# Optimization experiments

Hardware: AMD Instinct MI355X
Metric: run time of the kernel (lower is better)

The kernel has to match this reference:

```python
import jax, jax.numpy as jnp
import numpy as np

WIRES = 4

def _ry(theta):
    # theta: scalar or (N,) -> (2,2) or (N,2,2) complex64
    c = jnp.cos(theta / 2)
    s = jnp.sin(theta / 2)
    return jnp.stack([jnp.stack([c, -s], -1), jnp.stack([s, c], -1)], -2).astype(jnp.complex64)

def _rz(phi):
    e = jnp.exp(-0.5j * phi.astype(jnp.complex64))
    z = jnp.zeros_like(e)
    return jnp.stack([jnp.stack([e, z], -1), jnp.stack([z, jnp.conj(e)], -1)], -2)

def _apply(state, U, w):
    # state: (N,2,2,2,2); wire w lives on axis 1+w
    state = jnp.moveaxis(state, 1 + w, -1)
    if U.ndim == 2:
        state = jnp.einsum('ij,n...j->n...i', U, state)
    else:
        state = jnp.einsum('nij,n...j->n...i', U, state)
    return jnp.moveaxis(state, -1, 1 + w)

def _cnot(state, c, t):
    # flip target axis where control axis == 1
    s0, s1 = jnp.split(state, 2, axis=1 + c)
    s1 = jnp.flip(s1, axis=1 + t)
    return jnp.concatenate([s0, s1], axis=1 + c)

def _quanv(patches, q_params):
    # patches: (N,4) angles; q_params: (L,4,3). Batched 4-qubit statevector sim.
    N = patches.shape[0]
    state = jnp.zeros((N, 16), jnp.complex64).at[:, 0].set(1.0).reshape(N, 2, 2, 2, 2)
    num_layers = q_params.shape[0]
    for i in range(num_layers):
        for w in range(WIRES):
            state = _apply(state, _ry(patches[:, w]), w)
        for w in range(WIRES):
            state = _cnot(state, w, (w + 1) % WIRES)
        for w in range(WIRES):
            state = _apply(state, _rz(q_params[i, w, 0]), w)
            state = _apply(state, _ry(q_params[i, w, 1]), w)
            state = _apply(state, _rz(q_params[i, w, 2]), w)
    probs = jnp.abs(state) ** 2  # (N,2,2,2,2)
    zsign = jnp.array([1.0, -1.0], jnp.float32)
    ez = [jnp.sum(probs * zsign.reshape((1,) + (1,) * w + (2,) + (1,) * (WIRES - 1 - w)),
                  axis=(1, 2, 3, 4)) for w in range(WIRES)]
    return jnp.stack(ez, -1)  # (N,4) <Z_j> expectations

def setup_inputs() -> dict:
    key = jax.random.key(0)
    k1, k2, k3 = jax.random.split(key, 3)
    B = 1024
    x = jax.random.normal(k1, (B, 1, 28, 28), dtype=jnp.float32)
    q_params = jax.random.normal(k2, (3, 4, 3), dtype=jnp.float32)
    W = jax.random.normal(k3, (10, 784), dtype=jnp.float32) * 0.03
    b = jnp.zeros((10,), jnp.float32)
    return {"x": x, "q_params": q_params, "W": W, "b": b}

def reference(x, q_params, W, b):
    B = x.shape[0]
    # extract 2x2 patches in (row-block, col-block) order, each flattened row-major
    patches = x.reshape(B, 14, 2, 14, 2).transpose(0, 1, 3, 2, 4).reshape(B * 196, 4)
    feats = _quanv(patches, q_params).reshape(B, 196 * 4)  # cat order: patch-major, 4 wires each
    logits = feats @ W.T + b
    return jax.nn.log_softmax(logits, axis=-1)
```

## Files before the change

kernel.cpp:

```cpp
#include <hip/hip_runtime.h>
#include <math.h>


#define APPLY_RY(ST, cc, ss) do { \
  _Pragma("unroll") \
  for (int i = 0; i < 16; ++i) { \
    if (!(i & (ST))) { \
      float ar = sr[i], ai = si[i], br = sr[i + (ST)], bi = si[i + (ST)]; \
      sr[i]        = (cc) * ar - (ss) * br; \
      si[i]        = (cc) * ai - (ss) * bi; \
      sr[i + (ST)] = (ss) * ar + (cc) * br; \
      si[i + (ST)] = (ss) * ai + (cc) * bi; \
    } } } while (0)

#define APPLY_RZ(ST, cc, ss) do { \
  _Pragma("unroll") \
  for (int i = 0; i < 16; ++i) { \
    float m = (i & (ST)) ? (ss) : -(ss); \
    float ar = sr[i], ai = si[i]; \
    sr[i] = (cc) * ar - m * ai; \
    si[i] = (cc) * ai + m * ar; \
  } } while (0)

#define APPLY_CNOT(SC, ST) do { \
  _Pragma("unroll") \
  for (int i = 0; i < 16; ++i) { \
    if ((i & (SC)) && !(i & (ST))) { \
      float tr = sr[i], ti = si[i]; \
      sr[i] = sr[i + (ST)]; si[i] = si[i + (ST)]; \
      sr[i + (ST)] = tr;    si[i + (ST)] = ti; \
    } } } while (0)

__global__ __launch_bounds__(256) void quanv_fused_kernel(
    const float* __restrict__ x,
    const float* __restrict__ qp,
    const float* __restrict__ W,
    const float* __restrict__ bias,
    float* __restrict__ out,
    int L)
{
  const int n   = blockIdx.x;
  const int tid = threadIdx.x;
  const int p   = tid;

  __shared__ float qc[48], qs[48];
  const int nq = L * 12;
  if (tid < nq) {
    float s, c;
    sincosf(0.5f * qp[tid], &s, &c);
    qc[tid] = c; qs[tid] = s;
  }
  __syncthreads();

  float ez[4] = {0.f, 0.f, 0.f, 0.f};

  if (p < 196) {
    const int pr = p / 14, pcc = p % 14;
    const float* xb = x + (size_t)n * 784 + (2 * pr) * 28 + 2 * pcc;
    float ang0 = xb[0], ang1 = xb[1], ang2 = xb[28], ang3 = xb[29];
    float dc[4], ds[4];
    sincosf(0.5f * ang0, &ds[0], &dc[0]);
    sincosf(0.5f * ang1, &ds[1], &dc[1]);
    sincosf(0.5f * ang2, &ds[2], &dc[2]);
    sincosf(0.5f * ang3, &ds[3], &dc[3]);

    float sr[16], si[16];
#pragma unroll
    for (int i = 0; i < 16; ++i) { sr[i] = 0.f; si[i] = 0.f; }
    sr[0] = 1.f;

    for (int l = 0; l < L; ++l) {
      APPLY_RY(8, dc[0], ds[0]);
      APPLY_RY(4, dc[1], ds[1]);
      APPLY_RY(2, dc[2], ds[2]);
      APPLY_RY(1, dc[3], ds[3]);
      APPLY_CNOT(8, 4);
      APPLY_CNOT(4, 2);
      APPLY_CNOT(2, 1);
      APPLY_CNOT(1, 8);
      const int base = l * 12;
      APPLY_RZ(8, qc[base + 0],  qs[base + 0]);
      APPLY_RY(8, qc[base + 1],  qs[base + 1]);
      APPLY_RZ(8, qc[base + 2],  qs[base + 2]);
      APPLY_RZ(4, qc[base + 3],  qs[base + 3]);
      APPLY_RY(4, qc[base + 4],  qs[base + 4]);
      APPLY_RZ(4, qc[base + 5],  qs[base + 5]);
      APPLY_RZ(2, qc[base + 6],  qs[base + 6]);
      APPLY_RY(2, qc[base + 7],  qs[base + 7]);
      APPLY_RZ(2, qc[base + 8],  qs[base + 8]);
      APPLY_RZ(1, qc[base + 9],  qs[base + 9]);
      APPLY_RY(1, qc[base + 10], qs[base + 10]);
      APPLY_RZ(1, qc[base + 11], qs[base + 11]);
    }

#pragma unroll
    for (int i = 0; i < 16; ++i) {
      float pp = sr[i] * sr[i] + si[i] * si[i];
      ez[0] += (i & 8) ? -pp : pp;
      ez[1] += (i & 4) ? -pp : pp;
      ez[2] += (i & 2) ? -pp : pp;
      ez[3] += (i & 1) ? -pp : pp;
    }
  }

  float part[10];
#pragma unroll
  for (int c = 0; c < 10; ++c) part[c] = 0.f;
  if (p < 196) {
    const float4* Wv = (const float4*)W;
#pragma unroll
    for (int c = 0; c < 10; ++c) {
      float4 wc = Wv[c * 196 + p];
      part[c] = ez[0] * wc.x + ez[1] * wc.y + ez[2] * wc.z + ez[3] * wc.w;
    }
  }

  const int lane = tid & 63;
  const int wave = tid >> 6;
  __shared__ float red[4][10];
#pragma unroll
  for (int c = 0; c < 10; ++c) {
    float v = part[c];
#pragma unroll
    for (int off = 32; off > 0; off >>= 1) v += __shfl_down(v, off, 64);
    if (lane == 0) red[wave][c] = v;
  }
  __syncthreads();

  if (tid == 0) {
    float logits[10];
    float m = -1e30f;
#pragma unroll
    for (int c = 0; c < 10; ++c) {
      logits[c] = red[0][c] + red[1][c] + red[2][c] + red[3][c] + bias[c];
      m = fmaxf(m, logits[c]);
    }
    float sum = 0.f;
#pragma unroll
    for (int c = 0; c < 10; ++c) sum += expf(logits[c] - m);
    float lse = m + logf(sum);
#pragma unroll
    for (int c = 0; c < 10; ++c) out[(size_t)n * 10 + c] = logits[c] - lse;
  }
}

extern "C" void kernel_launch(void* const* d_in, const int* in_sizes, int n_in,
                              void* d_out, int out_size, void* d_ws, size_t ws_size,
                              hipStream_t stream) {
  const float* x    = (const float*)d_in[0];
  const float* qp   = (const float*)d_in[1];
  const float* W    = (const float*)d_in[2];
  const float* bias = (const float*)d_in[3];
  float* out        = (float*)d_out;

  const int B = in_sizes[0] / 784;
  const int L = in_sizes[1] / 12;

  quanv_fused_kernel<<<B, 256, 0, stream>>>(x, qp, W, bias, out, L);
}
```

Before: 89.63 us.

## Fuse RZ-RY-RZ into one SU(2) gate and specialize layer count at compile time

Each wire's RZ·RY·RZ sequence is combined into a single 2x2 unitary, computed once per block into shared memory, so every layer does one gate pass per wire instead of three. The first layer's data RY gates act on |0000> and are replaced by a closed-form product state. The kernel is templated on the layer count so the layer loop unrolls fully. Fast intrinsics (__sincosf, __expf, __logf) replace the precise math calls and input loads use float2. The fast intrinsics may lose accuracy for large input angles.

```diff
diff --git a/kernel.cpp b/kernel.cpp
--- a/kernel.cpp
+++ b/kernel.cpp
@@ -13,15 +13,6 @@
       si[i + (ST)] = (ss) * ai + (cc) * bi; \
     } } } while (0)
 
-#define APPLY_RZ(ST, cc, ss) do { \
-  _Pragma("unroll") \
-  for (int i = 0; i < 16; ++i) { \
-    float m = (i & (ST)) ? (ss) : -(ss); \
-    float ar = sr[i], ai = si[i]; \
-    sr[i] = (cc) * ar - m * ai; \
-    si[i] = (cc) * ai + m * ar; \
-  } } while (0)
-
 #define APPLY_CNOT(SC, ST) do { \
   _Pragma("unroll") \
   for (int i = 0; i < 16; ++i) { \
@@ -31,24 +22,62 @@
       sr[i + (ST)] = tr;    si[i + (ST)] = ti; \
     } } } while (0)
 
-__global__ __launch_bounds__(256) void quanv_fused_kernel(
+#define APPLY_U(ST, U0R, U0I, U1R, U1I) do { \
+  _Pragma("unroll") \
+  for (int i = 0; i < 16; ++i) { \
+    if (!(i & (ST))) { \
+      float ar = sr[i], ai = si[i], br = sr[i + (ST)], bi = si[i + (ST)]; \
+      sr[i]        =  (U0R) * ar - (U0I) * ai + (U1R) * br - (U1I) * bi; \
+      si[i]        =  (U0R) * ai + (U0I) * ar + (U1R) * bi + (U1I) * br; \
+      sr[i + (ST)] = -(U1R) * ar - (U1I) * ai + (U0R) * br + (U0I) * bi; \
+      si[i + (ST)] = -(U1R) * ai + (U1I) * ar + (U0R) * bi - (U0I) * br; \
+    } } } while (0)
+
+#define APPLY_U_LDS(ST, l, w) do { \
+  const float* u_ = &uu[((l) * 4 + (w)) * 4]; \
+  float u0r = u_[0], u0i = u_[1], u1r = u_[2], u1i = u_[3]; \
+  APPLY_U(ST, u0r, u0i, u1r, u1i); \
+} while (0)
+
+#define LAYER_TAIL(l) do { \
+  APPLY_CNOT(8, 4); APPLY_CNOT(4, 2); APPLY_CNOT(2, 1); APPLY_CNOT(1, 8); \
+  APPLY_U_LDS(8, l, 0); APPLY_U_LDS(4, l, 1); APPLY_U_LDS(2, l, 2); APPLY_U_LDS(1, l, 3); \
+} while (0)
+
+#define DATA_RY_ALL() do { \
+  APPLY_RY(8, dc[0], ds[0]); APPLY_RY(4, dc[1], ds[1]); \
+  APPLY_RY(2, dc[2], ds[2]); APPLY_RY(1, dc[3], ds[3]); \
+} while (0)
+
+template <int LC>
+__global__ __launch_bounds__(256, 4) void quanv_fused_kernel(
     const float* __restrict__ x,
     const float* __restrict__ qp,
     const float* __restrict__ W,
     const float* __restrict__ bias,
     float* __restrict__ out,
-    int L)
+    int Lrt)
 {
+  const int L = (LC > 0) ? LC : Lrt;
   const int n   = blockIdx.x;
   const int tid = threadIdx.x;
   const int p   = tid;
 
-  __shared__ float qc[48], qs[48];
-  const int nq = L * 12;
-  if (tid < nq) {
-    float s, c;
-    sincosf(0.5f * qp[tid], &s, &c);
-    qc[tid] = c; qs[tid] = s;
+  __shared__ float uu[8 * 16];
+  if (tid < 4 * L) {
+    const int l = tid >> 2, w = tid & 3;
+    const float p0 = qp[l * 12 + w * 3 + 0];
+    const float p1 = qp[l * 12 + w * 3 + 1];
+    const float p2 = qp[l * 12 + w * 3 + 2];
+    float c, s, ca, sa, cb, sb;
+    __sincosf(0.5f * p1, &s, &c);
+    __sincosf(0.5f * (p0 + p2), &sa, &ca);
+    __sincosf(0.5f * (p0 - p2), &sb, &cb);
+    float* u_ = &uu[(l * 4 + w) * 4];
+    u_[0] =  c * ca;
+    u_[1] = -c * sa;
+    u_[2] = -s * cb;
+    u_[3] = -s * sb;
   }
   __syncthreads();
 
@@ -56,41 +85,39 @@
 
   if (p < 196) {
     const int pr = p / 14, pcc = p % 14;
-    const float* xb = x + (size_t)n * 784 + (2 * pr) * 28 + 2 * pcc;
-    float ang0 = xb[0], ang1 = xb[1], ang2 = xb[28], ang3 = xb[29];
+    const float2* xb = (const float2*)(x + (size_t)n * 784 + (2 * pr) * 28 + 2 * pcc);
+    float2 top = xb[0], bot = xb[14];
     float dc[4], ds[4];
-    sincosf(0.5f * ang0, &ds[0], &dc[0]);
-    sincosf(0.5f * ang1, &ds[1], &dc[1]);
-    sincosf(0.5f * ang2, &ds[2], &dc[2]);
-    sincosf(0.5f * ang3, &ds[3], &dc[3]);
+    __sincosf(0.5f * top.x, &ds[0], &dc[0]);
+    __sincosf(0.5f * top.y, &ds[1], &dc[1]);
+    __sincosf(0.5f * bot.x, &ds[2], &dc[2]);
+    __sincosf(0.5f * bot.y, &ds[3], &dc[3]);
 
     float sr[16], si[16];
+
+    if (LC > 0) {
+      float p00 = dc[0] * dc[1], p01 = dc[0] * ds[1];
+      float p10 = ds[0] * dc[1], p11 = ds[0] * ds[1];
+      float q00 = dc[2] * dc[3], q01 = dc[2] * ds[3];
+      float q10 = ds[2] * dc[3], q11 = ds[2] * ds[3];
+      float hi[4] = {p00, p01, p10, p11};
+      float lo[4] = {q00, q01, q10, q11};
 #pragma unroll
-    for (int i = 0; i < 16; ++i) { sr[i] = 0.f; si[i] = 0.f; }
-    sr[0] = 1.f;
-
-    for (int l = 0; l < L; ++l) {
-      APPLY_RY(8, dc[0], ds[0]);
-      APPLY_RY(4, dc[1], ds[1]);
-      APPLY_RY(2, dc[2], ds[2]);
-      APPLY_RY(1, dc[3], ds[3]);
-      APPLY_CNOT(8, 4);
-      APPLY_CNOT(4, 2);
-      APPLY_CNOT(2, 1);
-      APPLY_CNOT(1, 8);
-      const int base = l * 12;
-      APPLY_RZ(8, qc[base + 0],  qs[base + 0]);
-      APPLY_RY(8, qc[base + 1],  qs[base + 1]);
-      APPLY_RZ(8, qc[base + 2],  qs[base + 2]);
-      APPLY_RZ(4, qc[base + 3],  qs[base + 3]);
-      APPLY_RY(4, qc[base + 4],  qs[base + 4]);
-      APPLY_RZ(4, qc[base + 5],  qs[base + 5]);
-      APPLY_RZ(2, qc[base + 6],  qs[base + 6]);
-      APPLY_RY(2, qc[base + 7],  qs[base + 7]);
-      APPLY_RZ(2, qc[base + 8],  qs[base + 8]);
-      APPLY_RZ(1, qc[base + 9],  qs[base + 9]);
-      APPLY_RY(1, qc[base + 10], qs[base + 10]);
-      APPLY_RZ(1, qc[base + 11], qs[base + 11]);
+      for (int i = 0; i < 16; ++i) { sr[i] = hi[i >> 2] * lo[i & 3]; si[i] = 0.f; }
+      LAYER_TAIL(0);
+#pragma unroll
+      for (int l = 1; l < ((LC > 0) ? LC : 1); ++l) {
+        DATA_RY_ALL();
+        LAYER_TAIL(l);
+      }
+    } else {
+#pragma unroll
+      for (int i = 0; i < 16; ++i) { sr[i] = 0.f; si[i] = 0.f; }
+      sr[0] = 1.f;
+      for (int l = 0; l < L; ++l) {
+        DATA_RY_ALL();
+        LAYER_TAIL(l);
+      }
     }
 
 #pragma unroll
@@ -137,8 +164,8 @@
     }
     float sum = 0.f;
 #pragma unroll
-    for (int c = 0; c < 10; ++c) sum += expf(logits[c] - m);
-    float lse = m + logf(sum);
+    for (int c = 0; c < 10; ++c) sum += __expf(logits[c] - m);
+    float lse = m + __logf(sum);
 #pragma unroll
     for (int c = 0; c < 10; ++c) out[(size_t)n * 10 + c] = logits[c] - lse;
   }
@@ -156,5 +183,11 @@
   const int B = in_sizes[0] / 784;
   const int L = in_sizes[1] / 12;
 
-  quanv_fused_kernel<<<B, 256, 0, stream>>>(x, qp, W, bias, out, L);
+  switch (L) {
+    case 1: quanv_fused_kernel<1><<<B, 256, 0, stream>>>(x, qp, W, bias, out, L); break;
+    case 2: quanv_fused_kernel<2><<<B, 256, 0, stream>>>(x, qp, W, bias, out, L); break;
+    case 3: quanv_fused_kernel<3><<<B, 256, 0, stream>>>(x, qp, W, bias, out, L); break;
+    case 4: quanv_fused_kernel<4><<<B, 256, 0, stream>>>(x, qp, W, bias, out, L); break;
+    default: quanv_fused_kernel<0><<<B, 256, 0, stream>>>(x, qp, W, bias, out, L); break;
+  }
 }
```

Result: faster. 81.99 us (-8.5%).
